# Performance work log

Hardware: AMD Instinct MI355X
Metric: run time of the kernel (lower is better)

Reference implementation:

```python
import jax, jax.numpy as jnp
from jax import lax
import numpy as np

VOCAB = 50257
EMB = 768
HID = [1024, 1024, 1024]
B, S = 2, 2048
LN_EPS_RNN = 1e-5   # torch default inside MinGRU layers
LN_EPS_OUT = 0.0    # NLPModel passes bias=False into LayerNorm's eps slot


def _layernorm(x, w, b, eps):
    mu = jnp.mean(x, axis=-1, keepdims=True)
    var = jnp.var(x, axis=-1, keepdims=True)
    return (x - mu) * lax.rsqrt(var + eps) * w + b


def _log_g(x):
    # log of g(x) = where(x>=0, x+0.5, sigmoid(x)), computed stably in log space
    return jnp.where(x >= 0, jnp.log(jax.nn.relu(x) + 0.5), -jax.nn.softplus(-x))


def _mingru_scan(gate, hidden, h0):
    # gate, hidden: [B,S,H]; h0: [B,1,H] (positive). Log-space parallel scan.
    log_coeffs = -jax.nn.softplus(gate)              # log(1-z)
    log_values = -jax.nn.softplus(-gate) + _log_g(hidden)  # log(z) + log g(h~)
    log_coeffs = jnp.pad(log_coeffs, ((0, 0), (1, 0), (0, 0)))
    log_values = jnp.concatenate([jnp.log(h0), log_values], axis=1)
    a_star = jnp.cumsum(log_coeffs, axis=1)
    log_h = a_star + lax.cumlogsumexp(log_values - a_star, axis=1)
    return jnp.exp(log_h)[:, 1:]                     # [B,S,H]


def setup_inputs() -> dict:
    key = jax.random.key(0)
    ks = jax.random.split(key, 8)
    inp = {}
    inp["ids"] = jax.random.randint(ks[0], (B, S), 0, VOCAB)
    inp["emb_W"] = jax.random.normal(ks[1], (VOCAB, EMB)) * 0.02
    dims = [EMB] + HID
    for l, (i, o) in enumerate(zip(dims[:-1], dims[1:])):
        inp[f"ln{l}_w"] = jnp.ones((i,))
        inp[f"ln{l}_b"] = jnp.zeros((i,))
        inp[f"gates{l}_W"] = jax.random.normal(jax.random.fold_in(key, 10 + l), (2 * o, i)) * (1.0 / np.sqrt(i))
    inp["res0_W"] = jax.random.normal(ks[2], (HID[0], EMB)) * (1.0 / np.sqrt(EMB))
    inp["lnf_w"] = jnp.ones((HID[-1],))
    inp["lnf_b"] = jnp.zeros((HID[-1],))
    inp["fc_W"] = jax.random.normal(ks[3], (VOCAB, HID[-1])) * 0.02
    inp["fc_b"] = jnp.zeros((VOCAB,))
    return inp


def reference(ids, emb_W, ln0_w, ln0_b, gates0_W, res0_W,
              ln1_w, ln1_b, gates1_W, ln2_w, ln2_b, gates2_W,
              lnf_w, lnf_b, fc_W, fc_b):
    x = emb_W[ids]                                   # [B,S,EMB]
    layers = [
        (ln0_w, ln0_b, gates0_W, res0_W),
        (ln1_w, ln1_b, gates1_W, None),
        (ln2_w, ln2_b, gates2_W, None),
    ]
    inp = x
    for ln_w, ln_b, gW, resW in layers:
        out_dim = gW.shape[0] // 2
        xn = _layernorm(inp, ln_w, ln_b, LN_EPS_RNN)
        gh = jnp.einsum('bsi,oi->bso', xn, gW)       # bias=False for minGRU
        gate, hidden = jnp.split(gh, 2, axis=-1)
        h0 = jnp.full((inp.shape[0], 1, out_dim), 0.5, dtype=inp.dtype)  # g(0)=0.5
        out = _mingru_scan(gate, hidden, h0)
        res = inp if resW is None else jnp.einsum('bsi,oi->bso', inp, resW)
        inp = out + res                              # residual, dropout=0
    x = _layernorm(inp, lnf_w, lnf_b, LN_EPS_OUT)
    logits = jnp.einsum('bsh,vh->bsv', x, fc_W) + fc_b
    return logits
```

## Files before the change

### kernel.cpp

```cpp
#include <hip/hip_runtime.h>
#include <stdint.h>
#include <stddef.h>


typedef __attribute__((ext_vector_type(4))) float f32x4;
typedef __attribute__((ext_vector_type(8))) short bf16x8;
typedef float f32x4u __attribute__((vector_size(16), aligned(4)));

__device__ __forceinline__ unsigned short f2bf(float f) {
  unsigned int u = __float_as_uint(f);
  u += 0x7FFFu + ((u >> 16) & 1u);
  return (unsigned short)(u >> 16);
}

__device__ __forceinline__ void gload16(const void* g, void* l) {
  __builtin_amdgcn_global_load_lds(
      (const __attribute__((address_space(1))) void*)g,
      (__attribute__((address_space(3))) void*)l, 16, 0, 0);
}

__global__ __launch_bounds__(256) void cvt_kernel(
    const float* __restrict__ in, unsigned short* __restrict__ out, int n8) {
  int i = blockIdx.x * 256 + threadIdx.x;
  int stride = gridDim.x * 256;
  for (; i < n8; i += stride) {
    const float4* p = (const float4*)in + (size_t)i * 2;
    float4 a = p[0], b = p[1];
    bf16x8 o;
    o[0] = (short)f2bf(a.x); o[1] = (short)f2bf(a.y);
    o[2] = (short)f2bf(a.z); o[3] = (short)f2bf(a.w);
    o[4] = (short)f2bf(b.x); o[5] = (short)f2bf(b.y);
    o[6] = (short)f2bf(b.z); o[7] = (short)f2bf(b.w);
    *(bf16x8*)(out + (size_t)i * 8) = o;
  }
}

__global__ __launch_bounds__(256) void embed_kernel(
    const int* __restrict__ ids, const float* __restrict__ embW,
    unsigned short* __restrict__ xbf) {
  int tok = blockIdx.x;
  int id = ids[tok];
  const float* src = embW + (size_t)id * 768;
  unsigned short* dst = xbf + (size_t)tok * 768;
  for (int j = threadIdx.x; j < 768; j += 256) dst[j] = f2bf(src[j]);
}

template <int BF16IN, int D>
__global__ __launch_bounds__(256) void ln_kernel(
    const void* __restrict__ xin, const float* __restrict__ w,
    const float* __restrict__ b, unsigned short* __restrict__ xout,
    float eps) {
  constexpr int NV = D / 256;
  int row = blockIdx.x;
  int tid = threadIdx.x;
  int lane = tid & 63, wid = tid >> 6;
  const float* xf = (const float*)xin;
  const unsigned short* xb = (const unsigned short*)xin;
  float vals[NV];
  float s = 0.f, ss = 0.f;
#pragma unroll
  for (int i = 0; i < NV; i++) {
    size_t idx = (size_t)row * D + i * 256 + tid;
    float v;
    if (BF16IN) {
      unsigned int u = ((unsigned int)xb[idx]) << 16;
      v = __uint_as_float(u);
    } else {
      v = xf[idx];
    }
    vals[i] = v;
    s += v;
    ss += v * v;
  }
  for (int off = 32; off; off >>= 1) {
    s += __shfl_down(s, off);
    ss += __shfl_down(ss, off);
  }
  __shared__ float red[8];
  if (lane == 0) { red[wid] = s; red[4 + wid] = ss; }
  __syncthreads();
  s = red[0] + red[1] + red[2] + red[3];
  ss = red[4] + red[5] + red[6] + red[7];
  constexpr float invD = 1.f / (float)D;
  float mu = s * invD;
  float var = ss * invD - mu * mu;
  float inv = rsqrtf(var + eps);
#pragma unroll
  for (int i = 0; i < NV; i++) {
    int col = i * 256 + tid;
    size_t idx = (size_t)row * D + col;
    float y = (vals[i] - mu) * inv * w[col] + b[col];
    xout[idx] = f2bf(y);
  }
}

template <int FINAL>
__global__ __launch_bounds__(256) void gemm_bt(
    const unsigned short* __restrict__ A, const unsigned short* __restrict__ B,
    float* __restrict__ C, const float* __restrict__ bias, int M, int N,
    int K) {
  __shared__ __align__(16) char smem[16896];
  unsigned short* lsA = (unsigned short*)smem;
  unsigned short* lsB = (unsigned short*)(smem + 8192);
  float* lsC = (float*)smem;

  const int tid = threadIdx.x;
  const int lane = tid & 63;
  const int wid = __builtin_amdgcn_readfirstlane(tid >> 6);
  const int row0 = blockIdx.y * 128;
  const int col0 = blockIdx.x * 128;

  const int srow = tid >> 2;
  const int skg = (tid & 3) * 8;

  int nB0 = col0 + srow, nB1 = col0 + 64 + srow;
  if (FINAL) { nB0 = min(nB0, N - 1); nB1 = min(nB1, N - 1); }
  const unsigned short* gA0 = A + (size_t)(row0 + srow) * K + skg;
  const unsigned short* gA1 = A + (size_t)(row0 + 64 + srow) * K + skg;
  const unsigned short* gB0 = B + (size_t)nB0 * K + skg;
  const unsigned short* gB1 = B + (size_t)nB1 * K + skg;

  char* ldsA0 = (char*)lsA + wid * 1024;
  char* ldsA1 = (char*)lsA + 4096 + wid * 1024;
  char* ldsB0 = (char*)lsB + wid * 1024;
  char* ldsB1 = (char*)lsB + 4096 + wid * 1024;

  const int wm = wid >> 1, wn = wid & 1;
  const unsigned short* pA = lsA + (wm * 64 + (lane & 15)) * 32 + (lane >> 4) * 8;
  const unsigned short* pB = lsB + (wn * 64 + (lane & 15)) * 32 + (lane >> 4) * 8;

  f32x4 acc[4][4] = {};

  for (int k0 = 0; k0 < K; k0 += 32) {
    gload16(gA0 + k0, ldsA0);
    gload16(gA1 + k0, ldsA1);
    gload16(gB0 + k0, ldsB0);
    gload16(gB1 + k0, ldsB1);
    __syncthreads();
    bf16x8 af[4], bfr[4];
#pragma unroll
    for (int i = 0; i < 4; i++) af[i] = *(const bf16x8*)(pA + i * 512);
#pragma unroll
    for (int i = 0; i < 4; i++) bfr[i] = *(const bf16x8*)(pB + i * 512);
#pragma unroll
    for (int i = 0; i < 4; i++)
#pragma unroll
      for (int j = 0; j < 4; j++)
        acc[i][j] = __builtin_amdgcn_mfma_f32_16x16x32_bf16(bfr[j], af[i],
                                                            acc[i][j], 0, 0, 0);
    __syncthreads();
  }

  const int mloc = lane & 15;
  const int ng = (lane >> 4) * 4;
  const int LDC = 132;
  const int trow = tid >> 5;
  const int tcol = (tid & 31) * 4;
#pragma unroll
  for (int c = 0; c < 4; c++) {
    if (wm == (c >> 1)) {
      const int i0 = 2 * (c & 1);
#pragma unroll
      for (int ii = 0; ii < 2; ii++)
#pragma unroll
        for (int j = 0; j < 4; j++)
          *(f32x4*)(lsC + (ii * 16 + mloc) * LDC + wn * 64 + j * 16 + ng) =
              acc[i0 + ii][j];
    }
    __syncthreads();
#pragma unroll
    for (int rr = 0; rr < 4; rr++) {
      const int r = rr * 8 + trow;
      const size_t gr = row0 + c * 32 + r;
      f32x4 v = *(const f32x4*)(lsC + r * LDC + tcol);
      if (!FINAL) {
        *(f32x4*)(C + gr * N + col0 + tcol) = v;
      } else {
        const int n0 = col0 + tcol;
        if (col0 + 128 <= N) {
          const f32x4u bv = *(const f32x4u*)(bias + n0);
          f32x4u o;
#pragma unroll
          for (int q = 0; q < 4; q++) o[q] = v[q] + bv[q];
          __builtin_nontemporal_store(o, (f32x4u*)(C + gr * N + n0));
        } else {
#pragma unroll
          for (int q = 0; q < 4; q++)
            if (n0 + q < N) C[gr * N + n0 + q] = v[q] + bias[n0 + q];
        }
      }
    }
    __syncthreads();
  }
}

__device__ __forceinline__ void gru_step(float gate, float hid, float& a,
                                         float& g) {
  a = 1.f / (1.f + expf(gate));
  g = (hid >= 0.f) ? (hid + 0.5f) : 1.f / (1.f + expf(-hid));
}

__global__ __launch_bounds__(256) void scan_compose(
    const float* __restrict__ gh, float* __restrict__ Acl,
    float* __restrict__ Vcl) {
  int ck = blockIdx.x;
  int hp = blockIdx.y * 256 + threadIdx.x;
  int b = hp >> 10, h = hp & 1023;
  const float* gb = gh + ((size_t)(b * 2048 + ck * 64)) * 2048 + h;
  float A = 1.f, V = 0.f;
  for (int t = 0; t < 64; t++) {
    float gate = gb[(size_t)t * 2048];
    float hid = gb[(size_t)t * 2048 + 1024];
    float a, g;
    gru_step(gate, hid, a, g);
    V = a * V + (1.f - a) * g;
    A *= a;
  }
  size_t i = (size_t)(b * 32 + ck) * 1024 + h;
  Acl[i] = A;
  Vcl[i] = V;
}

__global__ __launch_bounds__(256) void scan_prefix(
    const float* __restrict__ Acl, const float* __restrict__ Vcl,
    float* __restrict__ Hin) {
  int hp = blockIdx.x * 256 + threadIdx.x;
  int b = hp >> 10, h = hp & 1023;
  float hr = 0.5f;
  for (int ck = 0; ck < 32; ck++) {
    size_t i = (size_t)(b * 32 + ck) * 1024 + h;
    Hin[i] = hr;
    hr = Acl[i] * hr + Vcl[i];
  }
}

__global__ __launch_bounds__(256) void scan_emit(
    const float* __restrict__ gh, const float* __restrict__ Hin,
    const float* __restrict__ res, float* __restrict__ xout) {
  int ck = blockIdx.x;
  int hp = blockIdx.y * 256 + threadIdx.x;
  int b = hp >> 10, h = hp & 1023;
  const float* gb = gh + ((size_t)(b * 2048 + ck * 64)) * 2048 + h;
  const float* rb = res + ((size_t)(b * 2048 + ck * 64)) * 1024 + h;
  float* ob = xout + ((size_t)(b * 2048 + ck * 64)) * 1024 + h;
  float hc = Hin[(size_t)(b * 32 + ck) * 1024 + h];
  for (int t = 0; t < 64; t++) {
    float gate = gb[(size_t)t * 2048];
    float hid = gb[(size_t)t * 2048 + 1024];
    float a, g;
    gru_step(gate, hid, a, g);
    hc = a * hc + (1.f - a) * g;
    ob[(size_t)t * 1024] = hc + rb[(size_t)t * 1024];
  }
}

extern "C" void kernel_launch(void* const* d_in, const int* in_sizes, int n_in,
                              void* d_out, int out_size, void* d_ws,
                              size_t ws_size, hipStream_t stream) {
  (void)in_sizes; (void)n_in; (void)out_size; (void)ws_size;
  const int* ids = (const int*)d_in[0];
  const float* embW = (const float*)d_in[1];
  const float* ln0w = (const float*)d_in[2];
  const float* ln0b = (const float*)d_in[3];
  const float* g0W = (const float*)d_in[4];
  const float* ln1w = (const float*)d_in[5];
  const float* ln1b = (const float*)d_in[6];
  const float* g1W = (const float*)d_in[7];
  const float* ln2w = (const float*)d_in[8];
  const float* ln2b = (const float*)d_in[9];
  const float* g2W = (const float*)d_in[10];
  const float* r0W = (const float*)d_in[11];
  const float* lnfw = (const float*)d_in[12];
  const float* lnfb = (const float*)d_in[13];
  const float* fcW = (const float*)d_in[14];
  const float* fcb = (const float*)d_in[15];
  float* out = (float*)d_out;

  const int M = 4096;
  const int V = 50257;

  char* ws = (char*)d_ws;
  unsigned short* x_bf = (unsigned short*)(ws + 0);
  float* x_f = (float*)(ws + 6291456);
  unsigned short* xn_bf = (unsigned short*)(ws + 23068672);
  float* gh = (float*)(ws + 31457280);
  float* r0 = (float*)(ws + 65011712);
  float* Acl = (float*)(ws + 81788928);
  float* Vcl = (float*)(ws + 82051072);
  float* Hin = (float*)(ws + 82313216);
  unsigned short* gwbf = (unsigned short*)(ws + 82575360);
  unsigned short* rwbf = (unsigned short*)(ws + 86769664);
  unsigned short* fcwbf = (unsigned short*)(ws + 88342528);

  auto cvt = [&](const float* src, unsigned short* dst, int n) {
    int n8 = n / 8;
    int grid = min((n8 + 255) / 256, 2048);
    cvt_kernel<<<grid, 256, 0, stream>>>(src, dst, n8);
  };

  embed_kernel<<<M, 256, 0, stream>>>(ids, embW, x_bf);
  cvt(fcW, fcwbf, V * 1024);
  cvt(r0W, rwbf, 1024 * 768);

  cvt(g0W, gwbf, 2048 * 768);
  ln_kernel<1, 768><<<M, 256, 0, stream>>>(x_bf, ln0w, ln0b, xn_bf, 1e-5f);
  gemm_bt<0><<<dim3(16, 32), 256, 0, stream>>>(xn_bf, gwbf, gh, nullptr, M,
                                               2048, 768);
  gemm_bt<0><<<dim3(8, 32), 256, 0, stream>>>(x_bf, rwbf, r0, nullptr, M, 1024,
                                              768);
  scan_compose<<<dim3(32, 8), 256, 0, stream>>>(gh, Acl, Vcl);
  scan_prefix<<<8, 256, 0, stream>>>(Acl, Vcl, Hin);
  scan_emit<<<dim3(32, 8), 256, 0, stream>>>(gh, Hin, r0, x_f);

  cvt(g1W, gwbf, 2048 * 1024);
  ln_kernel<0, 1024><<<M, 256, 0, stream>>>(x_f, ln1w, ln1b, xn_bf, 1e-5f);
  gemm_bt<0><<<dim3(16, 32), 256, 0, stream>>>(xn_bf, gwbf, gh, nullptr, M,
                                               2048, 1024);
  scan_compose<<<dim3(32, 8), 256, 0, stream>>>(gh, Acl, Vcl);
  scan_prefix<<<8, 256, 0, stream>>>(Acl, Vcl, Hin);
  scan_emit<<<dim3(32, 8), 256, 0, stream>>>(gh, Hin, x_f, x_f);

  cvt(g2W, gwbf, 2048 * 1024);
  ln_kernel<0, 1024><<<M, 256, 0, stream>>>(x_f, ln2w, ln2b, xn_bf, 1e-5f);
  gemm_bt<0><<<dim3(16, 32), 256, 0, stream>>>(xn_bf, gwbf, gh, nullptr, M,
                                               2048, 1024);
  scan_compose<<<dim3(32, 8), 256, 0, stream>>>(gh, Acl, Vcl);
  scan_prefix<<<8, 256, 0, stream>>>(Acl, Vcl, Hin);
  scan_emit<<<dim3(32, 8), 256, 0, stream>>>(gh, Hin, x_f, x_f);

  ln_kernel<0, 1024><<<M, 256, 0, stream>>>(x_f, lnfw, lnfb, xn_bf, 0.0f);
  gemm_bt<1><<<dim3((V + 127) / 128, 32), 256, 0, stream>>>(xn_bf, fcwbf, out,
                                                            fcb, M, V, 1024);
}
```

Baseline: 1.059 ms.

## Add 256x256 double-buffered swizzled GEMM for the final vocab projection

Adds a new GEMM kernel for the large output projection (4096 x 50257 x 1024). It uses 512-thread blocks computing 256x256 tiles, a double-buffered LDS pipeline with XOR-swizzled layout, and staggered global-to-LDS prefetch interleaved with MFMA phases under raised priority. The grid is ordered so row tiles vary fastest, which lets consecutive blocks reuse the same weight columns. It targets the dominant logits GEMM, where the old 128x128 single-buffered kernel was limited by load latency and reuse. It uses 128KB of LDS, which lowers occupancy and costs more registers.

```diff
diff --git a/kernel.cpp b/kernel.cpp
--- a/kernel.cpp
+++ b/kernel.cpp
@@ -18,6 +18,8 @@
       (const __attribute__((address_space(1))) void*)g,
       (__attribute__((address_space(3))) void*)l, 16, 0, 0);
 }
+
+#define MEMFENCE asm volatile("" ::: "memory")
 
 __global__ __launch_bounds__(256) void cvt_kernel(
     const float* __restrict__ in, unsigned short* __restrict__ out, int n8) {
@@ -94,11 +96,9 @@
   }
 }
 
-template <int FINAL>
 __global__ __launch_bounds__(256) void gemm_bt(
     const unsigned short* __restrict__ A, const unsigned short* __restrict__ B,
-    float* __restrict__ C, const float* __restrict__ bias, int M, int N,
-    int K) {
+    float* __restrict__ C, int M, int N, int K) {
   __shared__ __align__(16) char smem[16896];
   unsigned short* lsA = (unsigned short*)smem;
   unsigned short* lsB = (unsigned short*)(smem + 8192);
@@ -113,12 +113,10 @@
   const int srow = tid >> 2;
   const int skg = (tid & 3) * 8;
 
-  int nB0 = col0 + srow, nB1 = col0 + 64 + srow;
-  if (FINAL) { nB0 = min(nB0, N - 1); nB1 = min(nB1, N - 1); }
   const unsigned short* gA0 = A + (size_t)(row0 + srow) * K + skg;
   const unsigned short* gA1 = A + (size_t)(row0 + 64 + srow) * K + skg;
-  const unsigned short* gB0 = B + (size_t)nB0 * K + skg;
-  const unsigned short* gB1 = B + (size_t)nB1 * K + skg;
+  const unsigned short* gB0 = B + (size_t)(col0 + srow) * K + skg;
+  const unsigned short* gB1 = B + (size_t)(col0 + 64 + srow) * K + skg;
 
   char* ldsA0 = (char*)lsA + wid * 1024;
   char* ldsA1 = (char*)lsA + 4096 + wid * 1024;
@@ -173,24 +171,166 @@
       const int r = rr * 8 + trow;
       const size_t gr = row0 + c * 32 + r;
       f32x4 v = *(const f32x4*)(lsC + r * LDC + tcol);
-      if (!FINAL) {
-        *(f32x4*)(C + gr * N + col0 + tcol) = v;
+      *(f32x4*)(C + gr * N + col0 + tcol) = v;
+    }
+    __syncthreads();
+  }
+}
+
+__global__ __launch_bounds__(512, 2) void gemm_bt256(
+    const unsigned short* __restrict__ A, const unsigned short* __restrict__ B,
+    float* __restrict__ C, const float* __restrict__ bias, int M, int N,
+    int K) {
+  __shared__ __align__(16) char smem[131072];
+  char* const aBuf0 = smem;
+  char* const bBuf0 = smem + 65536;
+
+  const int t = threadIdx.x;
+  const int l = t & 63;
+  const int w = __builtin_amdgcn_readfirstlane(t >> 6);
+  const int wm = w >> 2, wn = w & 3;
+  const int row0 = blockIdx.x * 256;
+  const int col0 = blockIdx.y * 256;
+
+  const int srow = t >> 3;
+  const int sg = ((t & 7) ^ (srow & 7)) * 8;
+  const unsigned short* aS0 = A + (size_t)(row0 + srow) * K + sg;
+  const unsigned short* aS1 = A + (size_t)(row0 + 64 + srow) * K + sg;
+  const unsigned short* aS2 = A + (size_t)(row0 + 128 + srow) * K + sg;
+  const unsigned short* aS3 = A + (size_t)(row0 + 192 + srow) * K + sg;
+  int br0 = min(col0 + srow, N - 1);
+  int br1 = min(col0 + 64 + srow, N - 1);
+  int br2 = min(col0 + 128 + srow, N - 1);
+  int br3 = min(col0 + 192 + srow, N - 1);
+  const unsigned short* bS0 = B + (size_t)br0 * K + sg;
+  const unsigned short* bS1 = B + (size_t)br1 * K + sg;
+  const unsigned short* bS2 = B + (size_t)br2 * K + sg;
+  const unsigned short* bS3 = B + (size_t)br3 * K + sg;
+  const int wOff = w * 1024;
+
+  const int aRowB = (wm * 128 + (l & 15)) * 128;
+  const int bRowB = (wn * 64 + (l & 15)) * 128;
+  const int gK0 = (((l >> 4)) ^ (l & 7)) * 16;
+  const int gK1 = ((4 + (l >> 4)) ^ (l & 7)) * 16;
+
+  f32x4 acc[8][4] = {};
+
+  gload16(aS0, aBuf0 + wOff);
+  gload16(aS1, aBuf0 + 8192 + wOff);
+  gload16(aS2, aBuf0 + 16384 + wOff);
+  gload16(aS3, aBuf0 + 24576 + wOff);
+  gload16(bS0, bBuf0 + wOff);
+  gload16(bS1, bBuf0 + 8192 + wOff);
+  gload16(bS2, bBuf0 + 16384 + wOff);
+  gload16(bS3, bBuf0 + 24576 + wOff);
+  asm volatile("s_waitcnt vmcnt(0)" ::: "memory");
+  __builtin_amdgcn_s_barrier();
+  MEMFENCE;
+
+  const int NT = K >> 6;
+  int cur = 0;
+  for (int kt = 0; kt < NT; ++kt) {
+    const int nxt = cur ^ 1;
+    const bool pre = (kt + 1 < NT);
+    const int kN = (kt + 1) << 6;
+    const char* aB = aBuf0 + cur * 32768;
+    const char* bB = bBuf0 + cur * 32768;
+    char* aN = aBuf0 + nxt * 32768;
+    char* bN = bBuf0 + nxt * 32768;
+
+    bf16x8 bf[4][2];
+    bf16x8 af[2][2];
+
+#define LOAD_A(FR0)                                                    \
+  af[0][0] = *(const bf16x8*)(aB + aRowB + (FR0) * 2048 + gK0);        \
+  af[0][1] = *(const bf16x8*)(aB + aRowB + (FR0) * 2048 + gK1);        \
+  af[1][0] = *(const bf16x8*)(aB + aRowB + ((FR0) + 1) * 2048 + gK0);  \
+  af[1][1] = *(const bf16x8*)(aB + aRowB + ((FR0) + 1) * 2048 + gK1);
+
+#define MFMA_PH(FR0)                                                      \
+  __builtin_amdgcn_s_setprio(1);                                          \
+  _Pragma("unroll") for (int ii = 0; ii < 2; ++ii) {                      \
+    _Pragma("unroll") for (int fc = 0; fc < 4; ++fc) {                    \
+      acc[(FR0) + ii][fc] = __builtin_amdgcn_mfma_f32_16x16x32_bf16(      \
+          bf[fc][0], af[ii][0], acc[(FR0) + ii][fc], 0, 0, 0);            \
+      acc[(FR0) + ii][fc] = __builtin_amdgcn_mfma_f32_16x16x32_bf16(      \
+          bf[fc][1], af[ii][1], acc[(FR0) + ii][fc], 0, 0, 0);            \
+    }                                                                     \
+  }                                                                       \
+  __builtin_amdgcn_s_setprio(0);
+
+#define BARRIER_ \
+  MEMFENCE;      \
+  __builtin_amdgcn_s_barrier(); \
+  MEMFENCE;
+
+#pragma unroll
+    for (int fc = 0; fc < 4; ++fc) {
+      bf[fc][0] = *(const bf16x8*)(bB + bRowB + fc * 2048 + gK0);
+      bf[fc][1] = *(const bf16x8*)(bB + bRowB + fc * 2048 + gK1);
+    }
+    LOAD_A(0);
+    if (pre) {
+      gload16(aS0 + kN, aN + wOff);
+      gload16(aS1 + kN, aN + 8192 + wOff);
+      gload16(aS2 + kN, aN + 16384 + wOff);
+    }
+    BARRIER_;
+    MFMA_PH(0);
+    BARRIER_;
+
+    LOAD_A(2);
+    if (pre) {
+      gload16(aS3 + kN, aN + 24576 + wOff);
+      gload16(bS0 + kN, bN + wOff);
+      gload16(bS1 + kN, bN + 8192 + wOff);
+    }
+    BARRIER_;
+    MFMA_PH(2);
+    BARRIER_;
+
+    LOAD_A(4);
+    if (pre) {
+      gload16(bS2 + kN, bN + 16384 + wOff);
+      gload16(bS3 + kN, bN + 24576 + wOff);
+    }
+    BARRIER_;
+    MFMA_PH(4);
+    BARRIER_;
+
+    LOAD_A(6);
+    BARRIER_;
+    MFMA_PH(6);
+    if (pre) asm volatile("s_waitcnt vmcnt(0)" ::: "memory");
+    BARRIER_;
+
+    cur = nxt;
+#undef LOAD_A
+#undef MFMA_PH
+#undef BARRIER_
+  }
+
+  const int mB = row0 + wm * 128 + (l & 15);
+  const int nB = col0 + wn * 64 + ((l >> 4) << 2);
+#pragma unroll
+  for (int fr = 0; fr < 8; ++fr) {
+    const size_t mRow = (size_t)(mB + fr * 16) * N;
+#pragma unroll
+    for (int fc = 0; fc < 4; ++fc) {
+      const int n0 = nB + fc * 16;
+      f32x4 v = acc[fr][fc];
+      if (n0 + 3 < N) {
+        const f32x4u bv = *(const f32x4u*)(bias + n0);
+        f32x4u o;
+#pragma unroll
+        for (int q = 0; q < 4; q++) o[q] = v[q] + bv[q];
+        __builtin_nontemporal_store(o, (f32x4u*)(C + mRow + n0));
       } else {
-        const int n0 = col0 + tcol;
-        if (col0 + 128 <= N) {
-          const f32x4u bv = *(const f32x4u*)(bias + n0);
-          f32x4u o;
-#pragma unroll
-          for (int q = 0; q < 4; q++) o[q] = v[q] + bv[q];
-          __builtin_nontemporal_store(o, (f32x4u*)(C + gr * N + n0));
-        } else {
-#pragma unroll
-          for (int q = 0; q < 4; q++)
-            if (n0 + q < N) C[gr * N + n0 + q] = v[q] + bias[n0 + q];
-        }
+#pragma unroll
+        for (int q = 0; q < 4; q++)
+          if (n0 + q < N) C[mRow + n0 + q] = v[q] + bias[n0 + q];
       }
     }
-    __syncthreads();
   }
 }
 
@@ -304,31 +444,27 @@
 
   cvt(g0W, gwbf, 2048 * 768);
   ln_kernel<1, 768><<<M, 256, 0, stream>>>(x_bf, ln0w, ln0b, xn_bf, 1e-5f);
-  gemm_bt<0><<<dim3(16, 32), 256, 0, stream>>>(xn_bf, gwbf, gh, nullptr, M,
-                                               2048, 768);
-  gemm_bt<0><<<dim3(8, 32), 256, 0, stream>>>(x_bf, rwbf, r0, nullptr, M, 1024,
-                                              768);
+  gemm_bt<<<dim3(16, 32), 256, 0, stream>>>(xn_bf, gwbf, gh, M, 2048, 768);
+  gemm_bt<<<dim3(8, 32), 256, 0, stream>>>(x_bf, rwbf, r0, M, 1024, 768);
   scan_compose<<<dim3(32, 8), 256, 0, stream>>>(gh, Acl, Vcl);
   scan_prefix<<<8, 256, 0, stream>>>(Acl, Vcl, Hin);
   scan_emit<<<dim3(32, 8), 256, 0, stream>>>(gh, Hin, r0, x_f);
 
   cvt(g1W, gwbf, 2048 * 1024);
   ln_kernel<0, 1024><<<M, 256, 0, stream>>>(x_f, ln1w, ln1b, xn_bf, 1e-5f);
-  gemm_bt<0><<<dim3(16, 32), 256, 0, stream>>>(xn_bf, gwbf, gh, nullptr, M,
-                                               2048, 1024);
+  gemm_bt<<<dim3(16, 32), 256, 0, stream>>>(xn_bf, gwbf, gh, M, 2048, 1024);
   scan_compose<<<dim3(32, 8), 256, 0, stream>>>(gh, Acl, Vcl);
   scan_prefix<<<8, 256, 0, stream>>>(Acl, Vcl, Hin);
   scan_emit<<<dim3(32, 8), 256, 0, stream>>>(gh, Hin, x_f, x_f);
 
   cvt(g2W, gwbf, 2048 * 1024);
   ln_kernel<0, 1024><<<M, 256, 0, stream>>>(x_f, ln2w, ln2b, xn_bf, 1e-5f);
-  gemm_bt<0><<<dim3(16, 32), 256, 0, stream>>>(xn_bf, gwbf, gh, nullptr, M,
-                                               2048, 1024);
+  gemm_bt<<<dim3(16, 32), 256, 0, stream>>>(xn_bf, gwbf, gh, M, 2048, 1024);
   scan_compose<<<dim3(32, 8), 256, 0, stream>>>(gh, Acl, Vcl);
   scan_prefix<<<8, 256, 0, stream>>>(Acl, Vcl, Hin);
   scan_emit<<<dim3(32, 8), 256, 0, stream>>>(gh, Hin, x_f, x_f);
 
   ln_kernel<0, 1024><<<M, 256, 0, stream>>>(x_f, lnfw, lnfb, xn_bf, 0.0f);
-  gemm_bt<1><<<dim3((V + 127) / 128, 32), 256, 0, stream>>>(xn_bf, fcwbf, out,
+  gemm_bt256<<<dim3(16, (V + 255) / 256), 512, 0, stream>>>(xn_bf, fcwbf, out,
                                                             fcb, M, V, 1024);
 }
```

Measured after the change: 1.414 ms. 1.34x slower.

## Add dedicated vocab-projection GEMM with K=64 tiles, XOR-swizzled LDS, row-major grid

Applied to the files above, without the earlier changes.

Splits the final logits GEMM into its own kernel. It loads 64-wide K slices per iteration into 32KB of LDS with an XOR swizzle to avoid bank conflicts. Each step issues two MFMAs per fragment pair, which halves the number of barriers and loop iterations. The grid is reordered so blocks sharing the same fc weight columns run adjacently, improving L2 reuse of the large weight matrix. The cost is higher LDS use per block, which may reduce occupancy.

```diff
diff --git a/kernel.cpp b/kernel.cpp
--- a/kernel.cpp
+++ b/kernel.cpp
@@ -94,11 +94,9 @@
   }
 }
 
-template <int FINAL>
 __global__ __launch_bounds__(256) void gemm_bt(
     const unsigned short* __restrict__ A, const unsigned short* __restrict__ B,
-    float* __restrict__ C, const float* __restrict__ bias, int M, int N,
-    int K) {
+    float* __restrict__ C, int M, int N, int K) {
   __shared__ __align__(16) char smem[16896];
   unsigned short* lsA = (unsigned short*)smem;
   unsigned short* lsB = (unsigned short*)(smem + 8192);
@@ -113,12 +111,10 @@
   const int srow = tid >> 2;
   const int skg = (tid & 3) * 8;
 
-  int nB0 = col0 + srow, nB1 = col0 + 64 + srow;
-  if (FINAL) { nB0 = min(nB0, N - 1); nB1 = min(nB1, N - 1); }
   const unsigned short* gA0 = A + (size_t)(row0 + srow) * K + skg;
   const unsigned short* gA1 = A + (size_t)(row0 + 64 + srow) * K + skg;
-  const unsigned short* gB0 = B + (size_t)nB0 * K + skg;
-  const unsigned short* gB1 = B + (size_t)nB1 * K + skg;
+  const unsigned short* gB0 = B + (size_t)(col0 + srow) * K + skg;
+  const unsigned short* gB1 = B + (size_t)(col0 + 64 + srow) * K + skg;
 
   char* ldsA0 = (char*)lsA + wid * 1024;
   char* ldsA1 = (char*)lsA + 4096 + wid * 1024;
@@ -173,21 +169,117 @@
       const int r = rr * 8 + trow;
       const size_t gr = row0 + c * 32 + r;
       f32x4 v = *(const f32x4*)(lsC + r * LDC + tcol);
-      if (!FINAL) {
-        *(f32x4*)(C + gr * N + col0 + tcol) = v;
+      *(f32x4*)(C + gr * N + col0 + tcol) = v;
+    }
+    __syncthreads();
+  }
+}
+
+__global__ __launch_bounds__(256) void gemm_final64(
+    const unsigned short* __restrict__ A, const unsigned short* __restrict__ B,
+    float* __restrict__ C, const float* __restrict__ bias, int M, int N,
+    int K) {
+  __shared__ __align__(16) char smem[32768];
+  char* const lsA = smem;
+  char* const lsB = smem + 16384;
+  float* const lsC = (float*)smem;
+
+  const int t = threadIdx.x;
+  const int l = t & 63;
+  const int w = __builtin_amdgcn_readfirstlane(t >> 6);
+  const int row0 = blockIdx.x * 128;
+  const int col0 = blockIdx.y * 128;
+
+  const int srow = t >> 3;
+  const int sg = ((t & 7) ^ (srow & 7)) * 8;
+  const unsigned short* gA0 = A + (size_t)(row0 + srow) * K + sg;
+  const unsigned short* gA1 = A + (size_t)(row0 + 32 + srow) * K + sg;
+  const unsigned short* gA2 = A + (size_t)(row0 + 64 + srow) * K + sg;
+  const unsigned short* gA3 = A + (size_t)(row0 + 96 + srow) * K + sg;
+  int b0 = min(col0 + srow, N - 1);
+  int b1 = min(col0 + 32 + srow, N - 1);
+  int b2 = min(col0 + 64 + srow, N - 1);
+  int b3 = min(col0 + 96 + srow, N - 1);
+  const unsigned short* gB0 = B + (size_t)b0 * K + sg;
+  const unsigned short* gB1 = B + (size_t)b1 * K + sg;
+  const unsigned short* gB2 = B + (size_t)b2 * K + sg;
+  const unsigned short* gB3 = B + (size_t)b3 * K + sg;
+  const int wOff = w * 1024;
+
+  const int wm = w >> 1, wn = w & 1;
+  const int aRowB = (wm * 64 + (l & 15)) * 128;
+  const int bRowB = (wn * 64 + (l & 15)) * 128;
+  const int gk0 = (((l >> 4)) ^ (l & 7)) * 16;
+  const int gk1 = ((4 + (l >> 4)) ^ (l & 7)) * 16;
+
+  f32x4 acc[4][4] = {};
+
+  for (int k0 = 0; k0 < K; k0 += 64) {
+    gload16(gA0 + k0, lsA + wOff);
+    gload16(gA1 + k0, lsA + 4096 + wOff);
+    gload16(gA2 + k0, lsA + 8192 + wOff);
+    gload16(gA3 + k0, lsA + 12288 + wOff);
+    gload16(gB0 + k0, lsB + wOff);
+    gload16(gB1 + k0, lsB + 4096 + wOff);
+    gload16(gB2 + k0, lsB + 8192 + wOff);
+    gload16(gB3 + k0, lsB + 12288 + wOff);
+    __syncthreads();
+    bf16x8 af[4][2], bfr[4][2];
+#pragma unroll
+    for (int i = 0; i < 4; i++) {
+      af[i][0] = *(const bf16x8*)(lsA + aRowB + i * 2048 + gk0);
+      af[i][1] = *(const bf16x8*)(lsA + aRowB + i * 2048 + gk1);
+    }
+#pragma unroll
+    for (int j = 0; j < 4; j++) {
+      bfr[j][0] = *(const bf16x8*)(lsB + bRowB + j * 2048 + gk0);
+      bfr[j][1] = *(const bf16x8*)(lsB + bRowB + j * 2048 + gk1);
+    }
+#pragma unroll
+    for (int i = 0; i < 4; i++)
+#pragma unroll
+      for (int j = 0; j < 4; j++) {
+        acc[i][j] = __builtin_amdgcn_mfma_f32_16x16x32_bf16(
+            bfr[j][0], af[i][0], acc[i][j], 0, 0, 0);
+        acc[i][j] = __builtin_amdgcn_mfma_f32_16x16x32_bf16(
+            bfr[j][1], af[i][1], acc[i][j], 0, 0, 0);
+      }
+    __syncthreads();
+  }
+
+  const int mloc = l & 15;
+  const int ng = (l >> 4) * 4;
+  const int LDC = 132;
+  const int trow = t >> 5;
+  const int tcol = (t & 31) * 4;
+#pragma unroll
+  for (int c = 0; c < 4; c++) {
+    if (wm == (c >> 1)) {
+      const int i0 = 2 * (c & 1);
+#pragma unroll
+      for (int ii = 0; ii < 2; ii++)
+#pragma unroll
+        for (int j = 0; j < 4; j++)
+          *(f32x4*)(lsC + (ii * 16 + mloc) * LDC + wn * 64 + j * 16 + ng) =
+              acc[i0 + ii][j];
+    }
+    __syncthreads();
+#pragma unroll
+    for (int rr = 0; rr < 4; rr++) {
+      const int r = rr * 8 + trow;
+      const size_t gr = row0 + c * 32 + r;
+      f32x4 v = *(const f32x4*)(lsC + r * LDC + tcol);
+      const int n0 = col0 + tcol;
+      if (col0 + 128 <= N) {
+        const f32x4u bv = *(const f32x4u*)(bias + n0);
+        f32x4u o;
+#pragma unroll
+        for (int q = 0; q < 4; q++) o[q] = v[q] + bv[q];
+        __builtin_nontemporal_store(o, (f32x4u*)(C + gr * N + n0));
       } else {
-        const int n0 = col0 + tcol;
-        if (col0 + 128 <= N) {
-          const f32x4u bv = *(const f32x4u*)(bias + n0);
-          f32x4u o;
-#pragma unroll
-          for (int q = 0; q < 4; q++) o[q] = v[q] + bv[q];
-          __builtin_nontemporal_store(o, (f32x4u*)(C + gr * N + n0));
-        } else {
-#pragma unroll
-          for (int q = 0; q < 4; q++)
-            if (n0 + q < N) C[gr * N + n0 + q] = v[q] + bias[n0 + q];
-        }
+#pragma unroll
+        for (int q = 0; q < 4; q++)
+          if (n0 + q < N) C[gr * N + n0 + q] = v[q] + bias[n0 + q];
       }
     }
     __syncthreads();
@@ -304,31 +396,27 @@
 
   cvt(g0W, gwbf, 2048 * 768);
   ln_kernel<1, 768><<<M, 256, 0, stream>>>(x_bf, ln0w, ln0b, xn_bf, 1e-5f);
-  gemm_bt<0><<<dim3(16, 32), 256, 0, stream>>>(xn_bf, gwbf, gh, nullptr, M,
-                                               2048, 768);
-  gemm_bt<0><<<dim3(8, 32), 256, 0, stream>>>(x_bf, rwbf, r0, nullptr, M, 1024,
-                                              768);
+  gemm_bt<<<dim3(16, 32), 256, 0, stream>>>(xn_bf, gwbf, gh, M, 2048, 768);
+  gemm_bt<<<dim3(8, 32), 256, 0, stream>>>(x_bf, rwbf, r0, M, 1024, 768);
   scan_compose<<<dim3(32, 8), 256, 0, stream>>>(gh, Acl, Vcl);
   scan_prefix<<<8, 256, 0, stream>>>(Acl, Vcl, Hin);
   scan_emit<<<dim3(32, 8), 256, 0, stream>>>(gh, Hin, r0, x_f);
 
   cvt(g1W, gwbf, 2048 * 1024);
   ln_kernel<0, 1024><<<M, 256, 0, stream>>>(x_f, ln1w, ln1b, xn_bf, 1e-5f);
-  gemm_bt<0><<<dim3(16, 32), 256, 0, stream>>>(xn_bf, gwbf, gh, nullptr, M,
-                                               2048, 1024);
+  gemm_bt<<<dim3(16, 32), 256, 0, stream>>>(xn_bf, gwbf, gh, M, 2048, 1024);
   scan_compose<<<dim3(32, 8), 256, 0, stream>>>(gh, Acl, Vcl);
   scan_prefix<<<8, 256, 0, stream>>>(Acl, Vcl, Hin);
   scan_emit<<<dim3(32, 8), 256, 0, stream>>>(gh, Hin, x_f, x_f);
 
   cvt(g2W, gwbf, 2048 * 1024);
   ln_kernel<0, 1024><<<M, 256, 0, stream>>>(x_f, ln2w, ln2b, xn_bf, 1e-5f);
-  gemm_bt<0><<<dim3(16, 32), 256, 0, stream>>>(xn_bf, gwbf, gh, nullptr, M,
-                                               2048, 1024);
+  gemm_bt<<<dim3(16, 32), 256, 0, stream>>>(xn_bf, gwbf, gh, M, 2048, 1024);
   scan_compose<<<dim3(32, 8), 256, 0, stream>>>(gh, Acl, Vcl);
   scan_prefix<<<8, 256, 0, stream>>>(Acl, Vcl, Hin);
   scan_emit<<<dim3(32, 8), 256, 0, stream>>>(gh, Hin, x_f, x_f);
 
   ln_kernel<0, 1024><<<M, 256, 0, stream>>>(x_f, lnfw, lnfb, xn_bf, 0.0f);
-  gemm_bt<1><<<dim3((V + 127) / 128, 32), 256, 0, stream>>>(xn_bf, fcwbf, out,
-                                                            fcb, M, V, 1024);
-}
+  gemm_final64<<<dim3(32, (V + 127) / 128), 256, 0, stream>>>(
+      xn_bf, fcwbf, out, fcb, M, V, 1024);
+}
```

New measurement: 925.8 us. 12.6% less time.
